# Performance work log

Hardware: AMD Instinct MI355X
Metric: run time of the kernel (lower is better)

The kernel has to match this reference:

```python
import jax, jax.numpy as jnp
import numpy as np

B, T, D = 16, 1024, 256
H, DK = 2, 128          # n_head, d_k = d_v = D // n_head
K = 5                   # conv kernel size
TEMP = float(np.sqrt(D))  # temperature = d_model ** 0.5


def mish(x):
    return x * jnp.tanh(jax.nn.softplus(x))


def setup_inputs() -> dict:
    key = jax.random.key(0)
    ks = jax.random.split(key, 16)
    s = 0.02
    p = lambda k, shp: jax.random.normal(k, shp, dtype=jnp.float32) * s
    inp = {
        'x': jax.random.normal(ks[0], (B, T, D), dtype=jnp.float32),
        'mask': jax.random.randint(ks[1], (B, T), 0, 2).astype(bool),
        # spectral MLP
        'W1': p(ks[2], (D, D)), 'b1': p(ks[3], (D,)),
        'W2': p(ks[4], (D, D)), 'b2': p(ks[5], (D,)),
        # two Conv1dGLU blocks: Conv1d(D -> 2D, k=5), torch layout [out,in,k]
        'cW1': p(ks[6], (2 * D, D, K)), 'cb1': p(ks[7], (2 * D,)),
        'cW2': p(ks[8], (2 * D, D, K)), 'cb2': p(ks[9], (2 * D,)),
        # attention projections (torch Linear: y = x @ W.T + b)
        'Wq': p(ks[10], (D, D)), 'bq': p(ks[11], (D,)),
        'Wk': p(ks[12], (D, D)), 'bk': p(ks[13], (D,)),
        'Wv': p(ks[14], (D, D)), 'bv': p(ks[15], (D,)),
        'Wo': p(jax.random.fold_in(key, 100), (D, D)),
        'bo': p(jax.random.fold_in(key, 101), (D,)),
        # final fc
        'Wf': p(jax.random.fold_in(key, 102), (D, D)),
        'bf': p(jax.random.fold_in(key, 103), (D,)),
    }
    return inp


def conv1d_glu(h, w, b):
    # h: [B, C, T]; w: [2C, C, K]; 'same' padding, GLU gate + residual
    y = jax.lax.conv_general_dilated(h, w, window_strides=(1,), padding=[(K // 2, K // 2)],
                                     dimension_numbers=('NCH', 'OIH', 'NCH'))
    y = y + b[None, :, None]
    a, g = jnp.split(y, 2, axis=1)
    return h + a * jax.nn.sigmoid(g)


def reference(x, mask, W1, b1, W2, b2, cW1, cb1, cW2, cb2,
              Wq, bq, Wk, bk, Wv, bv, Wo, bo, Wf, bf):
    # spectral: Linear + Mish (dropout is identity at inference)
    h = mish(x @ W1.T + b1)
    h = mish(h @ W2.T + b2)
    # temporal: two Conv1dGLU residual blocks over [B, C, T]
    h = h.transpose(0, 2, 1)
    h = conv1d_glu(h, cW1, cb1)
    h = conv1d_glu(h, cW2, cb2)
    h = h.transpose(0, 2, 1)
    # zero out padded frames
    h = jnp.where(mask[:, :, None], 0.0, h)
    residual = h
    # multi-head self-attention; mask hides padded keys
    q = (h @ Wq.T + bq).reshape(B, T, H, DK)
    k = (h @ Wk.T + bk).reshape(B, T, H, DK)
    v = (h @ Wv.T + bv).reshape(B, T, H, DK)
    attn = jnp.einsum('bqhd,bkhd->bhqk', q, k) / TEMP
    attn = jnp.where(mask[:, None, None, :], -jnp.inf, attn)
    attn = jax.nn.softmax(attn, axis=-1)
    out = jnp.einsum('bhqk,bkhd->bqhd', attn, v).reshape(B, T, D)
    h = out @ Wo.T + bo + residual
    # final projection + masked temporal average pool
    y = h @ Wf.T + bf
    len_ = (~mask).sum(axis=1, keepdims=True).astype(y.dtype)  # [B,1]
    y = jnp.where(mask[:, :, None], 0.0, y)
    w = y.sum(axis=1) / len_
    return w
```

## Files before the change

### kernel.cpp

```cpp
#include <hip/hip_runtime.h>
#include <hip/hip_bf16.h>
#include <math.h>


#define DEV __device__ __forceinline__

static constexpr int B_ = 16, T_ = 1024, D_ = 256;
static constexpr int N_ = B_ * T_;

typedef __attribute__((ext_vector_type(8))) short bf16x8;
typedef __attribute__((ext_vector_type(16))) float floatx16;

DEV float sigmoidf_(float x) { return 1.f / (1.f + __expf(-x)); }
DEV float mishf_(float x) {
  float u = __expf(fminf(x, 30.f));
  float t = u * (u + 2.f);
  return x * (t / (t + 2.f));
}
DEV ushort f2bf_(float x) {
  __hip_bfloat16 h = __float2bfloat16(x);
  return *(ushort*)&h;
}

__global__ __launch_bounds__(256) void prep_all_kernel(
    const unsigned* __restrict__ mraw,
    const float* __restrict__ W1, const float* __restrict__ W2,
    const float* __restrict__ Wq, const float* __restrict__ Wk,
    const float* __restrict__ Wv, const float* __restrict__ Wo,
    const float* __restrict__ cW1, const float* __restrict__ cW2,
    ushort* __restrict__ w1, ushort* __restrict__ w2,
    ushort* __restrict__ wqkv, ushort* __restrict__ wo,
    ushort* __restrict__ WtF1, ushort* __restrict__ WtF2,
    float* __restrict__ fmask, ushort* __restrict__ QF,
    ushort* __restrict__ KF, float* __restrict__ pooled) {
  int bid = blockIdx.x, tid = threadIdx.x;
  if (bid < 384) {
    int i = bid * 256 + tid;
    int widx = i >> 14, r = i & 16383;
    const float* src;
    ushort* dst;
    switch (widx) {
      case 0: src = W1; dst = w1; break;
      case 1: src = W2; dst = w2; break;
      case 2: src = Wq; dst = wqkv; break;
      case 3: src = Wk; dst = wqkv + 65536; break;
      case 4: src = Wv; dst = wqkv + 131072; break;
      default: src = Wo; dst = wo; break;
    }
    float4 v = ((const float4*)src)[r];
    ushort4 u;
    u.x = f2bf_(v.x); u.y = f2bf_(v.y); u.z = f2bf_(v.z); u.w = f2bf_(v.w);
    ((ushort4*)dst)[r] = u;
  } else if (bid < 1024) {
    int idx = (bid - 384) * 256 + tid;
    const float* cw = (idx < 81920) ? cW1 : cW2;
    ushort* dst = (idx < 81920) ? WtF1 : WtF2;
    int i8 = (idx < 81920) ? idx : idx - 81920;
    int i = i8 * 8;
    int half = (i >> 3) & 1, m31 = (i >> 4) & 31;
    int frag = i >> 9;
    int ks = frag & 1, c = (frag >> 1) & 7, tap = (frag >> 4) % 5,
        cot = frag / 80;
    int co = cot * 32 + m31;
    int cin0 = c * 32 + ks * 16 + half * 8;
    ushort u[8];
#pragma unroll
    for (int j = 0; j < 8; ++j)
      u[j] = f2bf_(cw[(size_t)(co * 256 + cin0 + j) * 5 + tap]);
    *(uint4*)&dst[i] = *(uint4*)u;
  } else {
    int isByte = 0, isFloat = 0;
    for (int i = 0; i < 16; ++i) {
      unsigned v = mraw[tid * 16 + i];
      if (v == 0x3F800000u) isFloat = 1;
      else if (v > 1u) isByte = 1;
    }
    __shared__ int sByte, sFloat;
    if (tid == 0) { sByte = 0; sFloat = 0; }
    __syncthreads();
    if (isByte) atomicOr(&sByte, 1);
    if (isFloat) atomicOr(&sFloat, 1);
    __syncthreads();
    int mode = sFloat ? 2 : (sByte ? 1 : 0);
    int mb = bid - 1024;
    int id = mb * 256 + tid;
    int bh = id >> 10, t = id & 1023, b = bh >> 1;
    int gidx = b * 1024 + t;
    unsigned mv;
    if (mode == 1) mv = ((const unsigned char*)mraw)[gidx];
    else           mv = mraw[gidx];
    float fm = (mv != 0u) ? 1.f : 0.f;
    if ((bh & 1) == 0) fmask[gidx] = fm;
    if (mb < 16) pooled[mb * 256 + tid] = 0.f;
    size_t qb = ((size_t)(bh * 32 + (t >> 5)) * 9 + 8) * 512 + (t & 31) * 16;
    QF[qb] = f2bf_(1.f);
#pragma unroll
    for (int j = 1; j < 16; ++j) QF[qb + j] = 0;
    size_t kb = ((size_t)(bh * 32 + (t >> 5)) * 9 + 8) * 512 + (t & 31) * 16;
    KF[kb] = (fm != 0.f) ? f2bf_(-60000.f) : (ushort)0;
#pragma unroll
    for (int j = 1; j < 16; ++j) KF[kb + j] = 0;
  }
}

template <int ACT, int RESID, int OMODE, int AF32>
__global__ __launch_bounds__(256, 4) void gemm_mfma_kernel(
    const void* __restrict__ Av, const ushort* __restrict__ W16,
    const float* __restrict__ bias, const float* __restrict__ resid,
    const float* __restrict__ fmask,
    float* __restrict__ outf, ushort* __restrict__ outb) {
  __shared__ __align__(16) ushort As[2][32 * 40];
  int tid = threadIdx.x;
  int w = tid >> 6, lane = tid & 63;
  int m31 = lane & 31, half = lane >> 5;
  int n0 = blockIdx.x * 32;
  int col = blockIdx.y * 128 + w * 32 + m31;
  const ushort* A16 = (const ushort*)Av;
  const float* A32 = (const float*)Av;

  floatx16 acc;
#pragma unroll
  for (int i = 0; i < 16; ++i) acc[i] = 0.f;

  {
    int row = tid >> 3, part = tid & 7;
    if (AF32) {
      float4 v = *(const float4*)&A32[(size_t)(n0 + row) * 256 + part * 4];
      ushort4 u;
      u.x = f2bf_(v.x); u.y = f2bf_(v.y); u.z = f2bf_(v.z); u.w = f2bf_(v.w);
      *(ushort4*)&As[0][row * 40 + part * 4] = u;
    } else {
      *(uint2*)&As[0][row * 40 + part * 4] =
          *(const uint2*)&A16[(size_t)(n0 + row) * 256 + part * 4];
    }
  }
  bf16x8 bn[2];
#pragma unroll
  for (int ks = 0; ks < 2; ++ks)
    bn[ks] = *(const bf16x8*)&W16[(size_t)col * 256 + ks * 16 + half * 8];

  for (int c = 0; c < 8; ++c) {
    __syncthreads();
    if (c < 7) {
      int k0 = (c + 1) * 32;
      int row = tid >> 3, part = tid & 7;
      if (AF32) {
        float4 v = *(const float4*)&A32[(size_t)(n0 + row) * 256 + k0 + part * 4];
        ushort4 u;
        u.x = f2bf_(v.x); u.y = f2bf_(v.y); u.z = f2bf_(v.z); u.w = f2bf_(v.w);
        *(ushort4*)&As[(c + 1) & 1][row * 40 + part * 4] = u;
      } else {
        *(uint2*)&As[(c + 1) & 1][row * 40 + part * 4] =
            *(const uint2*)&A16[(size_t)(n0 + row) * 256 + k0 + part * 4];
      }
    }
    bf16x8 bc[2] = {bn[0], bn[1]};
    if (c < 7) {
      int k0 = (c + 1) * 32;
#pragma unroll
      for (int ks = 0; ks < 2; ++ks)
        bn[ks] = *(const bf16x8*)&W16[(size_t)col * 256 + k0 + ks * 16 + half * 8];
    }
    const ushort* ab = As[c & 1];
#pragma unroll
    for (int ks = 0; ks < 2; ++ks) {
      bf16x8 af = *(const bf16x8*)&ab[m31 * 40 + ks * 16 + half * 8];
      acc = __builtin_amdgcn_mfma_f32_32x32x16_bf16(af, bc[ks], acc, 0, 0, 0);
    }
  }
  float bv = bias[col];
  if (OMODE == 3) {
    int b = n0 >> 10;
    float psum = 0.f;
#pragma unroll
    for (int reg = 0; reg < 16; ++reg) {
      int row = n0 + (reg & 3) + 8 * (reg >> 2) + 4 * half;
      float keep = (fmask[row] == 0.f) ? 1.f : 0.f;
      psum += keep * (acc[reg] + bv + resid[(size_t)row * 256 + col]);
    }
    atomicAdd(&outf[b * 256 + col], psum);
    return;
  }
#pragma unroll
  for (int reg = 0; reg < 16; ++reg) {
    int row = n0 + (reg & 3) + 8 * (reg >> 2) + 4 * half;
    float v = acc[reg] + bv;
    if (ACT == 1) v = mishf_(v);
    if (RESID) v += resid[(size_t)row * 256 + col];
    if (OMODE == 0) {
      outf[(size_t)row * 256 + col] = v;
    } else if (OMODE == 1) {
      outb[(size_t)row * 256 + col] = f2bf_(v);
    } else {
      outf[(size_t)row * 256 + col] = v;
      outb[(size_t)row * 256 + col] = f2bf_(v);
    }
  }
}

__global__ __launch_bounds__(256, 4) void qkv_mfma_kernel(
    const ushort* __restrict__ A16, const ushort* __restrict__ wqkv,
    const float* __restrict__ bq, const float* __restrict__ bk,
    const float* __restrict__ bv,
    ushort* __restrict__ QF, ushort* __restrict__ KF, ushort* __restrict__ VF) {
  __shared__ __align__(16) ushort As[2][32 * 40];
  __shared__ __align__(16) ushort Tw[4][32 * 40];
  int tid = threadIdx.x;
  int w = tid >> 6, lane = tid & 63;
  int m31 = lane & 31, half = lane >> 5;
  int n0 = blockIdx.x * 32;
  int by = blockIdx.z;
  const ushort* W16 = wqkv + (size_t)by * 65536;
  const float* bias = (by == 0) ? bq : (by == 1) ? bk : bv;
  int col = blockIdx.y * 128 + w * 32 + m31;

  floatx16 acc;
#pragma unroll
  for (int i = 0; i < 16; ++i) acc[i] = 0.f;

  {
    int row = tid >> 3, part = tid & 7;
    *(uint2*)&As[0][row * 40 + part * 4] =
        *(const uint2*)&A16[(size_t)(n0 + row) * 256 + part * 4];
  }
  bf16x8 bn[2];
#pragma unroll
  for (int ks = 0; ks < 2; ++ks)
    bn[ks] = *(const bf16x8*)&W16[(size_t)col * 256 + ks * 16 + half * 8];

  for (int c = 0; c < 8; ++c) {
    __syncthreads();
    if (c < 7) {
      int k0 = (c + 1) * 32;
      int row = tid >> 3, part = tid & 7;
      *(uint2*)&As[(c + 1) & 1][row * 40 + part * 4] =
          *(const uint2*)&A16[(size_t)(n0 + row) * 256 + k0 + part * 4];
    }
    bf16x8 bc[2] = {bn[0], bn[1]};
    if (c < 7) {
      int k0 = (c + 1) * 32;
#pragma unroll
      for (int ks = 0; ks < 2; ++ks)
        bn[ks] = *(const bf16x8*)&W16[(size_t)col * 256 + k0 + ks * 16 + half * 8];
    }
    const ushort* ab = As[c & 1];
#pragma unroll
    for (int ks = 0; ks < 2; ++ks) {
      bf16x8 af = *(const bf16x8*)&ab[m31 * 40 + ks * 16 + half * 8];
      acc = __builtin_amdgcn_mfma_f32_32x32x16_bf16(af, bc[ks], acc, 0, 0, 0);
    }
  }
  int b = n0 >> 10;
  float bvv = bias[col];
  int h = col >> 7, d127 = col & 127;
  int bh = b * 2 + h;
  if (by == 2) {
    int ctv = d127 >> 5, m31v = d127 & 31;
#pragma unroll
    for (int rg = 0; rg < 4; ++rg) {
      int t0 = (n0 & 1023) + 8 * rg + 4 * half;
      ushort4 u;
      u.x = f2bf_(acc[rg * 4 + 0] + bvv);
      u.y = f2bf_(acc[rg * 4 + 1] + bvv);
      u.z = f2bf_(acc[rg * 4 + 2] + bvv);
      u.w = f2bf_(acc[rg * 4 + 3] + bvv);
      size_t addr = ((size_t)(bh * 16 + (t0 >> 6)) * 16 +
                     ((t0 >> 4) & 3) * 4 + ctv) * 512 +
                    m31v * 16 + ((t0 >> 3) & 1) * 8 + (t0 & 7);
      *(ushort4*)&VF[addr] = u;
    }
  } else {
    float scale = (by == 0) ? 0.0625f : 1.f;
    ushort* tw = &Tw[w][0];
#pragma unroll
    for (int reg = 0; reg < 16; ++reg) {
      int brow = (reg & 3) + 8 * (reg >> 2) + 4 * half;
      tw[brow * 40 + m31] = f2bf_((acc[reg] + bvv) * scale);
    }
    ushort* dst = (by == 0) ? QF : KF;
    int tile9 = (bh * 32 + ((n0 & 1023) >> 5)) * 9;
    int c0 = (d127 & 127) >> 4;
    c0 = ((blockIdx.y * 128 + w * 32) & 127) >> 4;
    int tr = lane >> 1, hb = lane & 1;
#pragma unroll
    for (int cc = 0; cc < 2; ++cc) {
      uint4 v = *(const uint4*)&tw[tr * 40 + cc * 16 + hb * 8];
      *(uint4*)&dst[(size_t)(tile9 + c0 + cc) * 512 + lane * 8] = v;
    }
  }
}

template <int DO_MASK>
__global__ __launch_bounds__(256, 3) void conv_mfma_kernel(
    const ushort* __restrict__ H16, const float* __restrict__ Hf,
    const ushort* __restrict__ WtF, const float* __restrict__ cb,
    const float* __restrict__ fmask, float* __restrict__ outf,
    ushort* __restrict__ outb) {
  __shared__ __align__(16) ushort As[2][68 * 40];
  int tid = threadIdx.x;
  int w = tid >> 6, lane = tid & 63;
  int m31 = lane & 31, half = lane >> 5;
  int wr = w >> 1, wc = w & 1;
  int n0 = blockIdx.x * 64;
  int cg = blockIdx.y;
  int tbase = n0 & 1023;
  int acol = cg * 64 + wc * 32;
  int cotA = cg * 2 + wc, cotG = 8 + cg * 2 + wc;

  floatx16 acc[2];
#pragma unroll
  for (int ct = 0; ct < 2; ++ct)
#pragma unroll
    for (int i = 0; i < 16; ++i) acc[ct][i] = 0.f;

  for (int i = tid; i < 544; i += 256) {
    int row = i >> 3, part = i & 7;
    int t = tbase + row - 2;
    uint2 v = make_uint2(0u, 0u);
    if ((unsigned)t < 1024u)
      v = *(const uint2*)&H16[(size_t)(n0 + row - 2) * 256 + part * 4];
    *(uint2*)&As[0][row * 40 + part * 4] = v;
  }
  bf16x8 bn[2][2];
#pragma unroll
  for (int ks = 0; ks < 2; ++ks) {
    bn[ks][0] = *(const bf16x8*)&WtF[(size_t)(((cotA * 5 + 0) * 8 + 0) * 2 + ks) * 512 +
                                     m31 * 16 + half * 8];
    bn[ks][1] = *(const bf16x8*)&WtF[(size_t)(((cotG * 5 + 0) * 8 + 0) * 2 + ks) * 512 +
                                     m31 * 16 + half * 8];
  }

  for (int c = 0; c < 8; ++c) {
    __syncthreads();
    if (c < 7) {
      int k0 = (c + 1) * 32;
      for (int i = tid; i < 544; i += 256) {
        int row = i >> 3, part = i & 7;
        int t = tbase + row - 2;
        uint2 v = make_uint2(0u, 0u);
        if ((unsigned)t < 1024u)
          v = *(const uint2*)&H16[(size_t)(n0 + row - 2) * 256 + k0 + part * 4];
        *(uint2*)&As[(c + 1) & 1][row * 40 + part * 4] = v;
      }
    }
    const ushort* ab = As[c & 1];
#pragma unroll
    for (int tap = 0; tap < 5; ++tap) {
      bf16x8 bc[2][2];
#pragma unroll
      for (int ks = 0; ks < 2; ++ks)
#pragma unroll
        for (int ct = 0; ct < 2; ++ct) bc[ks][ct] = bn[ks][ct];
      int pc = c, pt = tap + 1;
      if (pt == 5) { pc = c + 1; pt = 0; }
      if (pc < 8) {
#pragma unroll
        for (int ks = 0; ks < 2; ++ks) {
          bn[ks][0] = *(const bf16x8*)&WtF[
              (size_t)(((cotA * 5 + pt) * 8 + pc) * 2 + ks) * 512 + m31 * 16 + half * 8];
          bn[ks][1] = *(const bf16x8*)&WtF[
              (size_t)(((cotG * 5 + pt) * 8 + pc) * 2 + ks) * 512 + m31 * 16 + half * 8];
        }
      }
#pragma unroll
      for (int ks = 0; ks < 2; ++ks) {
        bf16x8 af = *(const bf16x8*)&ab[(wr * 32 + m31 + tap) * 40 +
                                        ks * 16 + half * 8];
#pragma unroll
        for (int ct = 0; ct < 2; ++ct)
          acc[ct] = __builtin_amdgcn_mfma_f32_32x32x16_bf16(
              af, bc[ks][ct], acc[ct], 0, 0, 0);
      }
    }
  }
  int col = acol + m31;
  float ba = cb[col], bg = cb[256 + col];
#pragma unroll
  for (int reg = 0; reg < 16; ++reg) {
    int brow = wr * 32 + (reg & 3) + 8 * (reg >> 2) + 4 * half;
    int grow = n0 + brow;
    float a = acc[0][reg] + ba;
    float g = acc[1][reg] + bg;
    float v = Hf[(size_t)grow * 256 + col] + a * sigmoidf_(g);
    if (DO_MASK) {
      if (fmask[grow] != 0.f) v = 0.f;
    }
    outf[(size_t)grow * 256 + col] = v;
    outb[(size_t)grow * 256 + col] = f2bf_(v);
  }
}

__global__ __launch_bounds__(256, 3) void attn_mfma2_kernel(
    const ushort* __restrict__ QF, const ushort* __restrict__ KF,
    const ushort* __restrict__ VF, ushort* __restrict__ O) {
  __shared__ float Op[2][128][33];
  __shared__ float Ml[2][2][32];
  int tid = threadIdx.x;
  int w = tid >> 6, lane = tid & 63;
  int m31 = lane & 31, half = lane >> 5;
  int qt = w & 1, kh = w >> 1;
  int bh = blockIdx.x;
  int q0 = blockIdx.y * 64 + qt * 32;
  int lpos = m31 * 16 + half * 8;

  bf16x8 qe[9];
  {
    int qtile9 = (bh * 32 + (q0 >> 5)) * 9;
#pragma unroll
    for (int c = 0; c < 9; ++c)
      qe[c] = *(const bf16x8*)&QF[(size_t)(qtile9 + c) * 512 + lpos];
  }
  floatx16 oacc[4];
#pragma unroll
  for (int ct = 0; ct < 4; ++ct)
#pragma unroll
    for (int i = 0; i < 16; ++i) oacc[ct][i] = 0.f;
  float mi = -1e30f, li = 0.f;

  for (int it = 0; it < 8; ++it) {
    int ktb = kh * 512 + it * 64;
    int kfrag = (bh * 32 + (ktb >> 5)) * 9;
    int vtile = (bh * 16 + (ktb >> 6)) * 16;
    floatx16 s0, s1;
#pragma unroll
    for (int i = 0; i < 16; ++i) { s0[i] = 0.f; s1[i] = 0.f; }
#pragma unroll
    for (int c = 0; c < 9; ++c) {
      bf16x8 kf0 = *(const bf16x8*)&KF[(size_t)(kfrag + c) * 512 + lpos];
      bf16x8 kf1 = *(const bf16x8*)&KF[(size_t)(kfrag + 9 + c) * 512 + lpos];
      s0 = __builtin_amdgcn_mfma_f32_32x32x16_bf16(kf0, qe[c], s0, 0, 0, 0);
      s1 = __builtin_amdgcn_mfma_f32_32x32x16_bf16(kf1, qe[c], s1, 0, 0, 0);
    }
    float mloc = s0[0];
#pragma unroll
    for (int r = 1; r < 16; ++r) mloc = fmaxf(mloc, s0[r]);
#pragma unroll
    for (int r = 0; r < 16; ++r) mloc = fmaxf(mloc, s1[r]);
    float mt = fmaxf(mloc, __shfl_xor(mloc, 32));
    float mnew = fmaxf(mi, mt);
    float alpha = __expf(mi - mnew);
    bool dead = (mnew <= -3.0e4f);
    float sum = 0.f;
#pragma unroll
    for (int r = 0; r < 16; ++r) {
      float v0 = dead ? 0.f : __expf(s0[r] - mnew);
      float v1 = dead ? 0.f : __expf(s1[r] - mnew);
      s0[r] = v0; s1[r] = v1;
      sum += v0 + v1;
    }
    sum += __shfl_xor(sum, 32);
    li = li * alpha + sum;
    mi = mnew;
#pragma unroll
    for (int ct = 0; ct < 4; ++ct)
#pragma unroll
      for (int i = 0; i < 16; ++i) oacc[ct][i] *= alpha;
    bf16x8 pf[4];
#pragma unroll
    for (int sub = 0; sub < 2; ++sub) {
      float tx[16];
#pragma unroll
      for (int r = 0; r < 16; ++r)
        tx[r] = __shfl_xor(sub == 0 ? s0[r] : s1[r], 32);
#pragma unroll
      for (int s = 0; s < 2; ++s) {
        union { bf16x8 v; ushort u[8]; } pk;
#pragma unroll
        for (int j = 0; j < 8; ++j) {
          int base = s * 8;
          float own = (sub == 0) ? s0[base + j] : s1[base + j];
          float lo = (j < 4) ? own : tx[base + j - 4];
          float hi = (j < 4) ? tx[base + 4 + j] : own;
          pk.u[j] = f2bf_(half ? hi : lo);
        }
        pf[sub * 2 + s] = pk.v;
      }
    }
#pragma unroll
    for (int s2 = 0; s2 < 4; ++s2)
#pragma unroll
      for (int ct = 0; ct < 4; ++ct) {
        bf16x8 vf = *(const bf16x8*)&VF[(size_t)(vtile + s2 * 4 + ct) * 512 + lpos];
        oacc[ct] = __builtin_amdgcn_mfma_f32_32x32x16_bf16(
            vf, pf[s2], oacc[ct], 0, 0, 0);
      }
  }
  if (kh == 1) {
#pragma unroll
    for (int ct = 0; ct < 4; ++ct)
#pragma unroll
      for (int r = 0; r < 16; ++r) {
        int dv = ct * 32 + (r & 3) + 8 * (r >> 2) + 4 * half;
        Op[qt][dv][m31] = oacc[ct][r];
      }
    if (half == 0) { Ml[qt][0][m31] = mi; Ml[qt][1][m31] = li; }
  }
  __syncthreads();
  if (kh == 0) {
    float mB = Ml[qt][0][m31], lB = Ml[qt][1][m31];
    float m = fmaxf(mi, mB);
    float aA = __expf(mi - m), aB = __expf(mB - m);
    float l = li * aA + lB * aB;
    float inv = (l > 0.f) ? 1.f / l : 0.f;
    int b = bh >> 1, h = bh & 1;
    size_t rowbase = (size_t)(b * 1024 + q0 + m31) * 256 + h * 128;
#pragma unroll
    for (int ct = 0; ct < 4; ++ct)
#pragma unroll
      for (int rg = 0; rg < 4; ++rg) {
        int dv0 = ct * 32 + 8 * rg + 4 * half;
        ushort4 u;
        u.x = f2bf_((oacc[ct][rg * 4 + 0] * aA + Op[qt][dv0 + 0][m31] * aB) * inv);
        u.y = f2bf_((oacc[ct][rg * 4 + 1] * aA + Op[qt][dv0 + 1][m31] * aB) * inv);
        u.z = f2bf_((oacc[ct][rg * 4 + 2] * aA + Op[qt][dv0 + 2][m31] * aB) * inv);
        u.w = f2bf_((oacc[ct][rg * 4 + 3] * aA + Op[qt][dv0 + 3][m31] * aB) * inv);
        *(ushort4*)&O[rowbase + dv0] = u;
      }
  }
}

__global__ __launch_bounds__(256) void final_kernel(
    const float* __restrict__ pooled, const float* __restrict__ fmask,
    const float* __restrict__ Wf, const float* __restrict__ bf,
    float* __restrict__ out) {
  int b = blockIdx.x, j = threadIdx.x;
  __shared__ __align__(16) float p[256];
  __shared__ float red[256];
  p[j] = pooled[b * 256 + j];
  float c = 0.f;
  for (int i = 0; i < 4; ++i)
    c += (fmask[b * 1024 + i * 256 + j] == 0.f) ? 1.f : 0.f;
  red[j] = c;
  __syncthreads();
  for (int st = 128; st > 0; st >>= 1) {
    if (j < st) red[j] += red[j + st];
    __syncthreads();
  }
  float len = red[0];
  const float* wrow = Wf + (size_t)j * 256;
  float acc = 0.f;
  for (int d4 = 0; d4 < 64; ++d4) {
    float4 wv = ((const float4*)wrow)[d4];
    float4 pv = ((const float4*)p)[d4];
    acc += wv.x * pv.x + wv.y * pv.y + wv.z * pv.z + wv.w * pv.w;
  }
  float inv = (len > 0.f) ? 1.f / len : 0.f;
  out[b * 256 + j] = acc * inv + bf[j];
}

extern "C" void kernel_launch(void* const* d_in, const int* in_sizes, int n_in,
                              void* d_out, int out_size, void* d_ws, size_t ws_size,
                              hipStream_t stream) {
  const float* x      = (const float*)d_in[0];
  const unsigned* msk = (const unsigned*)d_in[1];
  const float* W1 = (const float*)d_in[2];
  const float* b1 = (const float*)d_in[3];
  const float* W2 = (const float*)d_in[4];
  const float* b2 = (const float*)d_in[5];
  const float* cW1 = (const float*)d_in[6];
  const float* cb1 = (const float*)d_in[7];
  const float* cW2 = (const float*)d_in[8];
  const float* cb2 = (const float*)d_in[9];
  const float* Wq = (const float*)d_in[10];
  const float* bq = (const float*)d_in[11];
  const float* Wk = (const float*)d_in[12];
  const float* bk = (const float*)d_in[13];
  const float* Wv = (const float*)d_in[14];
  const float* bv = (const float*)d_in[15];
  const float* Wo = (const float*)d_in[16];
  const float* bo = (const float*)d_in[17];
  const float* Wf = (const float*)d_in[18];
  const float* bf = (const float*)d_in[19];
  float* out = (float*)d_out;

  float* ws = (float*)d_ws;
  size_t ND = (size_t)N_ * D_;
  float* F0      = ws;
  float* F1      = F0 + ND;
  float* fmask   = F1 + ND;
  float* pooled  = fmask + N_;
  ushort* G0 = (ushort*)(pooled + 16 * 256);
  ushort* G1 = G0 + ND;
  ushort* QF = G1 + ND;
  ushort* KF = QF + (size_t)32 * 32 * 9 * 512;
  ushort* VF = KF + (size_t)32 * 32 * 9 * 512;
  ushort* w1_16 = VF + (size_t)32 * 16 * 16 * 512;
  ushort* w2_16 = w1_16 + 65536;
  ushort* wo_16 = w2_16 + 65536;
  ushort* wqkv  = wo_16 + 65536;
  ushort* WtF1  = wqkv + 3 * 65536;
  ushort* WtF2  = WtF1 + 655360;

  dim3 blk(256);
  prep_all_kernel<<<dim3(1152), blk, 0, stream>>>(
      msk, W1, W2, Wq, Wk, Wv, Wo, cW1, cW2,
      w1_16, w2_16, wqkv, wo_16, WtF1, WtF2, fmask, QF, KF, pooled);
  gemm_mfma_kernel<1, 0, 1, 1><<<dim3(512, 2), blk, 0, stream>>>(
      x, w1_16, b1, nullptr, nullptr, nullptr, G1);
  gemm_mfma_kernel<1, 0, 2, 0><<<dim3(512, 2), blk, 0, stream>>>(
      G1, w2_16, b2, nullptr, nullptr, F0, G0);
  conv_mfma_kernel<0><<<dim3(256, 4), blk, 0, stream>>>(
      G0, F0, WtF1, cb1, fmask, F1, G1);
  conv_mfma_kernel<1><<<dim3(256, 4), blk, 0, stream>>>(
      G1, F1, WtF2, cb2, fmask, F0, G0);
  qkv_mfma_kernel<<<dim3(512, 2, 3), blk, 0, stream>>>(
      G0, wqkv, bq, bk, bv, QF, KF, VF);
  attn_mfma2_kernel<<<dim3(32, 16), blk, 0, stream>>>(QF, KF, VF, G1);
  gemm_mfma_kernel<0, 1, 3, 0><<<dim3(512, 2), blk, 0, stream>>>(
      G1, wo_16, bo, F0, fmask, pooled, nullptr);
  final_kernel<<<dim3(16), blk, 0, stream>>>(pooled, fmask, Wf, bf, out);
}
```

Baseline: 322.0 us.

## Stage K/V tiles through double-buffered LDS in attention kernel

The attention kernel now cooperatively copies each 32-key K block and matching V block into a double-buffered shared-memory area, instead of having every wave load K/V fragments straight from global memory. Each wave handles 32 keys per iteration over 16 iterations rather than 64 keys over 8, and the next tile is staged after the current compute. This aims to cut redundant global traffic, since the two query-tile waves share the same K/V, and to overlap loads with MFMA work. In exchange it adds a barrier every iteration, uses about 70KB of LDS and lowers the occupancy target from 3 to 2 blocks per CU. The cross-wave output buffer now reuses the staging memory.

```diff
diff --git a/kernel.cpp b/kernel.cpp
--- a/kernel.cpp
+++ b/kernel.cpp
@@ -279,8 +279,7 @@
     }
     ushort* dst = (by == 0) ? QF : KF;
     int tile9 = (bh * 32 + ((n0 & 1023) >> 5)) * 9;
-    int c0 = (d127 & 127) >> 4;
-    c0 = ((blockIdx.y * 128 + w * 32) & 127) >> 4;
+    int c0 = ((blockIdx.y * 128 + w * 32) & 127) >> 4;
     int tr = lane >> 1, hb = lane & 1;
 #pragma unroll
     for (int cc = 0; cc < 2; ++cc) {
@@ -390,10 +389,10 @@
   }
 }
 
-__global__ __launch_bounds__(256, 3) void attn_mfma2_kernel(
+__global__ __launch_bounds__(256, 2) void attn_mfma4_kernel(
     const ushort* __restrict__ QF, const ushort* __restrict__ KF,
     const ushort* __restrict__ VF, ushort* __restrict__ O) {
-  __shared__ float Op[2][128][33];
+  __shared__ __align__(16) ushort Sm[2][17408];
   __shared__ float Ml[2][2][32];
   int tid = threadIdx.x;
   int w = tid >> 6, lane = tid & 63;
@@ -417,25 +416,45 @@
     for (int i = 0; i < 16; ++i) oacc[ct][i] = 0.f;
   float mi = -1e30f, li = 0.f;
 
-  for (int it = 0; it < 8; ++it) {
-    int ktb = kh * 512 + it * 64;
-    int kfrag = (bh * 32 + (ktb >> 5)) * 9;
-    int vtile = (bh * 16 + (ktb >> 6)) * 16;
-    floatx16 s0, s1;
-#pragma unroll
-    for (int i = 0; i < 16; ++i) { s0[i] = 0.f; s1[i] = 0.f; }
+  auto stage = [&](int it, int buf) {
+    const ushort* k0src = KF + (size_t)(bh * 32 + it) * 4608;
+    const ushort* k1src = KF + (size_t)(bh * 32 + 16 + it) * 4608;
+    const ushort* v0src =
+        VF + (size_t)((bh * 16 + (it >> 1)) * 16 + (it & 1) * 8) * 512;
+    const ushort* v1src =
+        VF + (size_t)((bh * 16 + 8 + (it >> 1)) * 16 + (it & 1) * 8) * 512;
+    auto copyc = [&](int c) {
+      const ushort* src;
+      int idx;
+      if (c < 576)       { src = k0src; idx = c; }
+      else if (c < 1152) { src = k1src; idx = c - 576; }
+      else if (c < 1664) { src = v0src; idx = c - 1152; }
+      else               { src = v1src; idx = c - 1664; }
+      uint4 v = *(const uint4*)(src + idx * 8);
+      *(uint4*)&Sm[buf][c * 8] = v;
+    };
+#pragma unroll
+    for (int k = 0; k < 8; ++k) copyc(tid + k * 256);
+    if (tid < 128) copyc(2048 + tid);
+  };
+
+  stage(0, 0);
+  for (int it = 0; it < 16; ++it) {
+    __syncthreads();
+    int buf = it & 1;
+    const ushort* Kb = &Sm[buf][kh * 4608];
+    const ushort* Vb = &Sm[buf][9216 + kh * 4096];
+    floatx16 s0;
+#pragma unroll
+    for (int i = 0; i < 16; ++i) s0[i] = 0.f;
 #pragma unroll
     for (int c = 0; c < 9; ++c) {
-      bf16x8 kf0 = *(const bf16x8*)&KF[(size_t)(kfrag + c) * 512 + lpos];
-      bf16x8 kf1 = *(const bf16x8*)&KF[(size_t)(kfrag + 9 + c) * 512 + lpos];
-      s0 = __builtin_amdgcn_mfma_f32_32x32x16_bf16(kf0, qe[c], s0, 0, 0, 0);
-      s1 = __builtin_amdgcn_mfma_f32_32x32x16_bf16(kf1, qe[c], s1, 0, 0, 0);
+      bf16x8 kf = *(const bf16x8*)&Kb[c * 512 + lpos];
+      s0 = __builtin_amdgcn_mfma_f32_32x32x16_bf16(kf, qe[c], s0, 0, 0, 0);
     }
     float mloc = s0[0];
 #pragma unroll
     for (int r = 1; r < 16; ++r) mloc = fmaxf(mloc, s0[r]);
-#pragma unroll
-    for (int r = 0; r < 16; ++r) mloc = fmaxf(mloc, s1[r]);
     float mt = fmaxf(mloc, __shfl_xor(mloc, 32));
     float mnew = fmaxf(mi, mt);
     float alpha = __expf(mi - mnew);
@@ -443,10 +462,9 @@
     float sum = 0.f;
 #pragma unroll
     for (int r = 0; r < 16; ++r) {
-      float v0 = dead ? 0.f : __expf(s0[r] - mnew);
-      float v1 = dead ? 0.f : __expf(s1[r] - mnew);
-      s0[r] = v0; s1[r] = v1;
-      sum += v0 + v1;
+      float v = dead ? 0.f : __expf(s0[r] - mnew);
+      s0[r] = v;
+      sum += v;
     }
     sum += __shfl_xor(sum, 32);
     li = li * alpha + sum;
@@ -455,43 +473,41 @@
     for (int ct = 0; ct < 4; ++ct)
 #pragma unroll
       for (int i = 0; i < 16; ++i) oacc[ct][i] *= alpha;
-    bf16x8 pf[4];
-#pragma unroll
-    for (int sub = 0; sub < 2; ++sub) {
-      float tx[16];
-#pragma unroll
-      for (int r = 0; r < 16; ++r)
-        tx[r] = __shfl_xor(sub == 0 ? s0[r] : s1[r], 32);
-#pragma unroll
-      for (int s = 0; s < 2; ++s) {
-        union { bf16x8 v; ushort u[8]; } pk;
-#pragma unroll
-        for (int j = 0; j < 8; ++j) {
-          int base = s * 8;
-          float own = (sub == 0) ? s0[base + j] : s1[base + j];
-          float lo = (j < 4) ? own : tx[base + j - 4];
-          float hi = (j < 4) ? tx[base + 4 + j] : own;
-          pk.u[j] = f2bf_(half ? hi : lo);
-        }
-        pf[sub * 2 + s] = pk.v;
-      }
-    }
-#pragma unroll
-    for (int s2 = 0; s2 < 4; ++s2)
+    float tx[16];
+#pragma unroll
+    for (int r = 0; r < 16; ++r) tx[r] = __shfl_xor(s0[r], 32);
+    bf16x8 pf[2];
+#pragma unroll
+    for (int s = 0; s < 2; ++s) {
+      union { bf16x8 v; ushort u[8]; } pk;
+#pragma unroll
+      for (int j = 0; j < 8; ++j) {
+        int base = s * 8;
+        float own = s0[base + j];
+        float lo = (j < 4) ? own : tx[base + j - 4];
+        float hi = (j < 4) ? tx[base + 4 + j] : own;
+        pk.u[j] = f2bf_(half ? hi : lo);
+      }
+      pf[s] = pk.v;
+    }
+#pragma unroll
+    for (int s2 = 0; s2 < 2; ++s2)
 #pragma unroll
       for (int ct = 0; ct < 4; ++ct) {
-        bf16x8 vf = *(const bf16x8*)&VF[(size_t)(vtile + s2 * 4 + ct) * 512 + lpos];
+        bf16x8 vf = *(const bf16x8*)&Vb[(s2 * 4 + ct) * 512 + lpos];
         oacc[ct] = __builtin_amdgcn_mfma_f32_32x32x16_bf16(
             vf, pf[s2], oacc[ct], 0, 0, 0);
       }
-  }
+    if (it < 15) stage(it + 1, (it + 1) & 1);
+  }
+  float* Opf = (float*)&Sm[0][0];
   if (kh == 1) {
 #pragma unroll
     for (int ct = 0; ct < 4; ++ct)
 #pragma unroll
       for (int r = 0; r < 16; ++r) {
         int dv = ct * 32 + (r & 3) + 8 * (r >> 2) + 4 * half;
-        Op[qt][dv][m31] = oacc[ct][r];
+        Opf[(qt * 128 + dv) * 33 + m31] = oacc[ct][r];
       }
     if (half == 0) { Ml[qt][0][m31] = mi; Ml[qt][1][m31] = li; }
   }
@@ -510,10 +526,10 @@
       for (int rg = 0; rg < 4; ++rg) {
         int dv0 = ct * 32 + 8 * rg + 4 * half;
         ushort4 u;
-        u.x = f2bf_((oacc[ct][rg * 4 + 0] * aA + Op[qt][dv0 + 0][m31] * aB) * inv);
-        u.y = f2bf_((oacc[ct][rg * 4 + 1] * aA + Op[qt][dv0 + 1][m31] * aB) * inv);
-        u.z = f2bf_((oacc[ct][rg * 4 + 2] * aA + Op[qt][dv0 + 2][m31] * aB) * inv);
-        u.w = f2bf_((oacc[ct][rg * 4 + 3] * aA + Op[qt][dv0 + 3][m31] * aB) * inv);
+        u.x = f2bf_((oacc[ct][rg * 4 + 0] * aA + Opf[(qt * 128 + dv0 + 0) * 33 + m31] * aB) * inv);
+        u.y = f2bf_((oacc[ct][rg * 4 + 1] * aA + Opf[(qt * 128 + dv0 + 1) * 33 + m31] * aB) * inv);
+        u.z = f2bf_((oacc[ct][rg * 4 + 2] * aA + Opf[(qt * 128 + dv0 + 2) * 33 + m31] * aB) * inv);
+        u.w = f2bf_((oacc[ct][rg * 4 + 3] * aA + Opf[(qt * 128 + dv0 + 3) * 33 + m31] * aB) * inv);
         *(ushort4*)&O[rowbase + dv0] = u;
       }
   }
@@ -605,7 +621,7 @@
       G1, F1, WtF2, cb2, fmask, F0, G0);
   qkv_mfma_kernel<<<dim3(512, 2, 3), blk, 0, stream>>>(
       G0, wqkv, bq, bk, bv, QF, KF, VF);
-  attn_mfma2_kernel<<<dim3(32, 16), blk, 0, stream>>>(QF, KF, VF, G1);
+  attn_mfma4_kernel<<<dim3(32, 16), blk, 0, stream>>>(QF, KF, VF, G1);
   gemm_mfma_kernel<0, 1, 3, 0><<<dim3(512, 2), blk, 0, stream>>>(
       G1, wo_16, bo, F0, fmask, pooled, nullptr);
   final_kernel<<<dim3(16), blk, 0, stream>>>(pooled, fmask, Wf, bf, out);
```

After: 284.0 us. 1.13x faster.
